# Kernel tuning notes

Hardware: AMD Instinct MI355X
Metric: run time of the kernel (lower is better)

Reference implementation:

```python
import jax, jax.numpy as jnp
import numpy as np

N_NODES = 100000
N_EDGES = 640000
IN_CH, HID_CH, OUT_CH = 256, 128, 64


def setup_inputs() -> dict:
    key = jax.random.key(0)
    ks = jax.random.split(key, 6)
    x = jax.random.normal(ks[0], (N_NODES, IN_CH), dtype=jnp.float32)
    edge_index = jax.random.randint(ks[1], (2, N_EDGES), 0, N_NODES, dtype=jnp.int32)
    # Glorot-style init for GCNConv weights
    W1 = jax.random.normal(ks[2], (IN_CH, HID_CH), dtype=jnp.float32) * (1.0 / np.sqrt(IN_CH))
    W_mu = jax.random.normal(ks[3], (HID_CH, OUT_CH), dtype=jnp.float32) * (1.0 / np.sqrt(HID_CH))
    W_logvar = jax.random.normal(ks[4], (HID_CH, OUT_CH), dtype=jnp.float32) * (1.0 / np.sqrt(HID_CH))
    return {
        "x": x,
        "edge_index": edge_index,
        "W1": W1,
        "b1": jnp.zeros((HID_CH,), jnp.float32),
        "W_mu": W_mu,
        "b_mu": jnp.zeros((OUT_CH,), jnp.float32),
        "W_logvar": W_logvar,
        "b_logvar": jnp.zeros((OUT_CH,), jnp.float32),
    }


def reference(x, edge_index, W1, b1, W_mu, b_mu, W_logvar, b_logvar):
    N = x.shape[0]
    # PyG GCNConv default: add self-loops, symmetric normalization D^-1/2 A_hat D^-1/2
    loops = jnp.arange(N, dtype=edge_index.dtype)
    src = jnp.concatenate([edge_index[0], loops])  # [E+N]
    dst = jnp.concatenate([edge_index[1], loops])  # [E+N]
    deg = jax.ops.segment_sum(jnp.ones_like(src, dtype=x.dtype), dst, num_segments=N)
    dinv = jax.lax.rsqrt(deg)  # deg >= 1 due to self-loops
    norm = dinv[src] * dinv[dst]  # [E+N]

    def gcn_conv(h, W, b):
        h = h @ W                                   # [N, d_out]
        msg = h[src] * norm[:, None]                # gather + scale  [E+N, d_out]
        out = jax.ops.segment_sum(msg, dst, num_segments=N)  # scatter-add
        return out + b

    h = jax.nn.relu(gcn_conv(x, W1, b1))
    mu = gcn_conv(h, W_mu, b_mu)
    logvar = gcn_conv(h, W_logvar, b_logvar)
    return (mu, logvar)
```

## Files before the change

### kernel.cpp

```cpp
#include <hip/hip_runtime.h>
#include <hip/hip_bf16.h>

#define N_NODES 100000
#define E_EDGES 640000

typedef __attribute__((ext_vector_type(8))) short short8;
typedef __attribute__((ext_vector_type(4))) float float4v;

__device__ __forceinline__ float bf2f(unsigned int u16) {
    union { unsigned int i; float f; } c; c.i = u16 << 16; return c.f;
}
__device__ __forceinline__ unsigned short f2bf(float f) {
    union { float f; unsigned int i; } c; c.f = f;
    unsigned int x = c.i;
    unsigned int r = (x + 0x7fffu + ((x >> 16) & 1u)) >> 16;
    return (unsigned short)r;
}

#define ASYNC16(g, l)                                                          \
    __builtin_amdgcn_global_load_lds(                                          \
        (const __attribute__((address_space(1))) void*)(g),                    \
        (__attribute__((address_space(3))) void*)(l), 16, 0, 0)

#define WS_HIST    0
#define WS_CURSOR  524288
#define WS_OFFS    1048576
#define WS_DINV    1572864
#define WS_BSUMS   2097152
#define WS_EIDX    2621440
#define WS_WP1     7864320
#define WS_WP2     7929856
#define WS_H0      7962624
#define WS_H       33562624

__global__ __launch_bounds__(256) void k_hist(const int* __restrict__ dst, int* __restrict__ hist) {
    int e = blockIdx.x * 256 + threadIdx.x;
    if (e < E_EDGES) atomicAdd(&hist[dst[e]], 1);
}

__global__ __launch_bounds__(256) void k_scan1(const int* __restrict__ hist,
                                               int* __restrict__ offs,
                                               int* __restrict__ bsums,
                                               float* __restrict__ dinv) {
    __shared__ int sd[256];
    int t = threadIdx.x;
    int base = blockIdx.x * 1024 + t * 4;
    int v[4];
#pragma unroll
    for (int j = 0; j < 4; ++j) v[j] = (base + j < N_NODES) ? hist[base + j] : 0;
#pragma unroll
    for (int j = 0; j < 4; ++j)
        if (base + j < N_NODES) dinv[base + j] = rsqrtf((float)(v[j] + 1));
    int s = v[0] + v[1] + v[2] + v[3];
    sd[t] = s;
    __syncthreads();
    for (int d = 1; d < 256; d <<= 1) {
        int x = (t >= d) ? sd[t - d] : 0;
        __syncthreads();
        sd[t] += x;
        __syncthreads();
    }
    int excl = sd[t] - s;
    if (t == 255) bsums[blockIdx.x] = sd[255];
    int run = excl;
#pragma unroll
    for (int j = 0; j < 4; ++j) {
        if (base + j < N_NODES) offs[base + j] = run;
        run += v[j];
    }
}

__global__ __launch_bounds__(128) void k_scan2(int* __restrict__ bsums, int nb) {
    __shared__ int sd[128];
    int t = threadIdx.x;
    int v = (t < nb) ? bsums[t] : 0;
    sd[t] = v;
    __syncthreads();
    for (int d = 1; d < 128; d <<= 1) {
        int x = (t >= d) ? sd[t - d] : 0;
        __syncthreads();
        sd[t] += x;
        __syncthreads();
    }
    if (t < nb) bsums[t] = sd[t] - v;
}

__global__ __launch_bounds__(256) void k_scan3(int* __restrict__ offs, const int* __restrict__ bsums) {
    int i = blockIdx.x * 256 + threadIdx.x;
    if (i < N_NODES) offs[i] += bsums[i >> 10];
}

__global__ __launch_bounds__(256) void k_fill(const int* __restrict__ src, const int* __restrict__ dst,
                                              const int* __restrict__ offs, int* __restrict__ cursor,
                                              const float* __restrict__ dinv,
                                              int2* __restrict__ eidx) {
    int e = blockIdx.x * 256 + threadIdx.x;
    if (e < E_EDGES) {
        int s = src[e], d = dst[e];
        int p = offs[d] + atomicAdd(&cursor[d], 1);
        int2 v;
        v.x = s;
        v.y = __float_as_int(dinv[s] * dinv[d]);
        eidx[p] = v;
    }
}

__global__ __launch_bounds__(256) void k_pack(const float* __restrict__ W1,
                                              const float* __restrict__ Wmu,
                                              const float* __restrict__ Wlv,
                                              unsigned short* __restrict__ Wp1,
                                              unsigned short* __restrict__ Wp2) {
    int i = blockIdx.x * 256 + threadIdx.x;
    if (i < 256 * 128) {
        int k = i >> 7, n = i & 127;
        Wp1[n * 256 + k] = f2bf(W1[i]);
    }
    if (i < 128 * 128) {
        int k = i >> 7, n = i & 127;
        float w = (n < 64) ? Wmu[k * 64 + n] : Wlv[k * 64 + (n - 64)];
        Wp2[n * 128 + k] = f2bf(w);
    }
}

__global__ __launch_bounds__(256) void k_mgemm1(const float* __restrict__ A,
                                                const unsigned short* __restrict__ Bpack,
                                                unsigned short* __restrict__ out) {
    __shared__ float As[128 * 32];
    __shared__ unsigned short Bs[128 * 40];
    int tid = threadIdx.x;
    int row0 = blockIdx.x * 128;
    int wave = tid >> 6, lane = tid & 63;
    int c = lane & 15, q = lane >> 4;
    int wrow = (wave >> 1) * 64, wcol = (wave & 1) * 64;

    float4v acc[4][4];
#pragma unroll
    for (int i = 0; i < 4; ++i)
#pragma unroll
        for (int j = 0; j < 4; ++j) acc[i][j] = (float4v){0.f, 0.f, 0.f, 0.f};

    int srow = tid >> 1;
    int shalf = (tid & 1) * 16;

    for (int k0 = 0; k0 < 256; k0 += 32) {
        const unsigned short* bsrc = Bpack + (size_t)srow * 256 + k0 + shalf;
        short8 b0 = *(const short8*)(bsrc);
        short8 b1 = *(const short8*)(bsrc + 8);
#pragma unroll
        for (int t = 0; t < 4; ++t) {
            int S = (t * 4 + wave) * 64 + lane;
            int row = S >> 3, j = S & 7;
            int kq = j ^ (row & 7);
            const float* g = A + (size_t)(row0 + row) * 256 + k0 + kq * 4;
            float* ldst = As + (t * 4 + wave) * 256;
            if (row0 + row < N_NODES) ASYNC16(g, ldst);
        }
        *(short8*)(&Bs[srow * 40 + shalf])     = b0;
        *(short8*)(&Bs[srow * 40 + shalf + 8]) = b1;
        __syncthreads();

        short8 af[4], bfr[4];
#pragma unroll
        for (int mt = 0; mt < 4; ++mt) {
            int r = wrow + mt * 16 + c;
            int j0 = (q * 2) ^ (r & 7);
            float4v fa = *(const float4v*)(&As[r * 32 + j0 * 4]);
            float4v fb = *(const float4v*)(&As[r * 32 + (j0 ^ 1) * 4]);
            short8 s;
#pragma unroll
            for (int jj = 0; jj < 4; ++jj) s[jj]     = (short)f2bf(fa[jj]);
#pragma unroll
            for (int jj = 0; jj < 4; ++jj) s[4 + jj] = (short)f2bf(fb[jj]);
            af[mt] = s;
        }
#pragma unroll
        for (int nt = 0; nt < 4; ++nt)
            bfr[nt] = *(const short8*)(&Bs[(wcol + nt * 16 + c) * 40 + q * 8]);
#pragma unroll
        for (int mt = 0; mt < 4; ++mt)
#pragma unroll
            for (int nt = 0; nt < 4; ++nt)
                acc[mt][nt] = __builtin_amdgcn_mfma_f32_16x16x32_bf16(af[mt], bfr[nt], acc[mt][nt], 0, 0, 0);
        __syncthreads();
    }

#pragma unroll
    for (int mt = 0; mt < 4; ++mt) {
#pragma unroll
        for (int i = 0; i < 4; ++i) {
            int row = row0 + wrow + mt * 16 + q * 4 + i;
            if (row >= N_NODES) continue;
#pragma unroll
            for (int nt = 0; nt < 4; ++nt) {
                int cc = wcol + nt * 16 + c;
                out[(size_t)row * 128 + cc] = f2bf(acc[mt][nt][i]);
            }
        }
    }
}

__global__ __launch_bounds__(256) void k_mgemm2(const unsigned short* __restrict__ A,
                                                const unsigned short* __restrict__ Bpack,
                                                const float* __restrict__ bias0,
                                                const float* __restrict__ bias1,
                                                float* __restrict__ out) {
    constexpr int LDT = 40;
    __shared__ unsigned short As[128 * LDT];
    __shared__ unsigned short Bs[128 * LDT];
    int tid = threadIdx.x;
    int row0 = blockIdx.x * 128;
    int wave = tid >> 6, lane = tid & 63;
    int c = lane & 15, q = lane >> 4;
    int wrow = (wave >> 1) * 64, wcol = (wave & 1) * 64;

    float4v acc[4][4];
#pragma unroll
    for (int i = 0; i < 4; ++i)
#pragma unroll
        for (int j = 0; j < 4; ++j) acc[i][j] = (float4v){0.f, 0.f, 0.f, 0.f};

    int srow = tid >> 1, shalf = (tid & 1) * 16;
    const short8 zed = {0, 0, 0, 0, 0, 0, 0, 0};

    for (int k0 = 0; k0 < 128; k0 += 32) {
        const unsigned short* bsrc = Bpack + (size_t)srow * 128 + k0 + shalf;
        short8 b0 = *(const short8*)(bsrc);
        short8 b1 = *(const short8*)(bsrc + 8);
        int grow = row0 + srow;
        short8 a0 = zed, a1 = zed;
        if (grow < N_NODES) {
            const unsigned short* asrc = A + (size_t)grow * 128 + k0 + shalf;
            a0 = *(const short8*)(asrc);
            a1 = *(const short8*)(asrc + 8);
        }
        *(short8*)(&Bs[srow * LDT + shalf])     = b0;
        *(short8*)(&Bs[srow * LDT + shalf + 8]) = b1;
        *(short8*)(&As[srow * LDT + shalf])     = a0;
        *(short8*)(&As[srow * LDT + shalf + 8]) = a1;
        __syncthreads();

        short8 af[4], bfr[4];
#pragma unroll
        for (int mt = 0; mt < 4; ++mt)
            af[mt] = *(const short8*)(&As[(wrow + mt * 16 + c) * LDT + q * 8]);
#pragma unroll
        for (int nt = 0; nt < 4; ++nt)
            bfr[nt] = *(const short8*)(&Bs[(wcol + nt * 16 + c) * LDT + q * 8]);
#pragma unroll
        for (int mt = 0; mt < 4; ++mt)
#pragma unroll
            for (int nt = 0; nt < 4; ++nt)
                acc[mt][nt] = __builtin_amdgcn_mfma_f32_16x16x32_bf16(af[mt], bfr[nt], acc[mt][nt], 0, 0, 0);
        __syncthreads();
    }

#pragma unroll
    for (int mt = 0; mt < 4; ++mt) {
#pragma unroll
        for (int i = 0; i < 4; ++i) {
            int row = row0 + wrow + mt * 16 + q * 4 + i;
            if (row >= N_NODES) continue;
#pragma unroll
            for (int nt = 0; nt < 4; ++nt) {
                int cc = wcol + nt * 16 + c;
                float v = acc[mt][nt][i];
                if (cc < 64) out[(size_t)row * 64 + cc] = v + bias0[cc];
                else out[(size_t)N_NODES * 64 + (size_t)row * 64 + (cc - 64)] = v + bias1[cc - 64];
            }
        }
    }
}

template <int BIAS_RELU>
__global__ __launch_bounds__(256) void k_agg(const unsigned int* __restrict__ in,
                                             unsigned int* __restrict__ out,
                                             const float* __restrict__ dinv,
                                             const int2* __restrict__ eidx,
                                             const int* __restrict__ offs,
                                             const int* __restrict__ cnt,
                                             const float* __restrict__ bias) {
    int wid = (blockIdx.x * 256 + threadIdx.x) >> 6;
    if (wid >= N_NODES) return;
    int l = threadIdx.x & 63;
    float di = dinv[wid];
    unsigned int u = in[(size_t)wid * 64 + l];
    float sc = di * di;
    float ax = sc * bf2f(u & 0xffffu);
    float ay = sc * bf2f(u >> 16);
    if (BIAS_RELU) { ax += bias[2 * l]; ay += bias[2 * l + 1]; }
    int start = offs[wid];
    int n = cnt[wid];

    for (int base = 0; base < n; base += 64) {
        int m = min(n - base, 64);
        int sreg = 0; float wreg = 0.f;
        if (l < m) {
            int2 ev = eidx[start + base + l];
            sreg = ev.x;
            wreg = __int_as_float(ev.y);
        }
        int e = 0;
        for (; e + 4 <= m; e += 4) {
            int s0 = __shfl(sreg, e),     s1 = __shfl(sreg, e + 1);
            int s2 = __shfl(sreg, e + 2), s3 = __shfl(sreg, e + 3);
            float w0 = __shfl(wreg, e),     w1 = __shfl(wreg, e + 1);
            float w2 = __shfl(wreg, e + 2), w3 = __shfl(wreg, e + 3);
            unsigned int u0 = in[(size_t)s0 * 64 + l];
            unsigned int u1 = in[(size_t)s1 * 64 + l];
            unsigned int u2 = in[(size_t)s2 * 64 + l];
            unsigned int u3 = in[(size_t)s3 * 64 + l];
            ax += w0 * bf2f(u0 & 0xffffu); ay += w0 * bf2f(u0 >> 16);
            ax += w1 * bf2f(u1 & 0xffffu); ay += w1 * bf2f(u1 >> 16);
            ax += w2 * bf2f(u2 & 0xffffu); ay += w2 * bf2f(u2 >> 16);
            ax += w3 * bf2f(u3 & 0xffffu); ay += w3 * bf2f(u3 >> 16);
        }
        for (; e < m; ++e) {
            int s0 = __shfl(sreg, e);
            float w0 = __shfl(wreg, e);
            unsigned int u0 = in[(size_t)s0 * 64 + l];
            ax += w0 * bf2f(u0 & 0xffffu); ay += w0 * bf2f(u0 >> 16);
        }
    }
    if (BIAS_RELU) { ax = fmaxf(ax, 0.f); ay = fmaxf(ay, 0.f); }
    out[(size_t)wid * 64 + l] = (unsigned int)f2bf(ax) | ((unsigned int)f2bf(ay) << 16);
}

extern "C" void kernel_launch(void* const* d_in, const int* in_sizes, int n_in,
                              void* d_out, int out_size, void* d_ws, size_t ws_size,
                              hipStream_t stream) {
    const float* x    = (const float*)d_in[0];
    const int*   ei   = (const int*)d_in[1];
    const float* W1   = (const float*)d_in[2];
    const float* b1   = (const float*)d_in[3];
    const float* Wmu  = (const float*)d_in[4];
    const float* bmu  = (const float*)d_in[5];
    const float* Wlv  = (const float*)d_in[6];
    const float* blv  = (const float*)d_in[7];
    float* outp = (float*)d_out;

    const int* src = ei;
    const int* dst = ei + E_EDGES;

    char* ws = (char*)d_ws;
    int*            hist   = (int*)(ws + WS_HIST);
    int*            cursor = (int*)(ws + WS_CURSOR);
    int*            offs   = (int*)(ws + WS_OFFS);
    float*          dinv   = (float*)(ws + WS_DINV);
    int*            bsums  = (int*)(ws + WS_BSUMS);
    int2*           eidx   = (int2*)(ws + WS_EIDX);
    unsigned short* Wp1    = (unsigned short*)(ws + WS_WP1);
    unsigned short* Wp2    = (unsigned short*)(ws + WS_WP2);
    unsigned short* h0     = (unsigned short*)(ws + WS_H0);
    unsigned short* h      = (unsigned short*)(ws + WS_H);

    const int NB_N = (N_NODES + 255) / 256;
    const int NB_E = (E_EDGES + 255) / 256;
    const int NB_S = (N_NODES + 1023) / 1024;
    const int NB_G = (N_NODES + 127) / 128;

    hipMemsetAsync(ws + WS_HIST, 0, 1048576, stream);
    k_hist<<<NB_E, 256, 0, stream>>>(dst, hist);
    k_scan1<<<NB_S, 256, 0, stream>>>(hist, offs, bsums, dinv);
    k_scan2<<<1, 128, 0, stream>>>(bsums, NB_S);
    k_scan3<<<NB_N, 256, 0, stream>>>(offs, bsums);
    k_fill<<<NB_E, 256, 0, stream>>>(src, dst, offs, cursor, dinv, eidx);
    k_pack<<<128, 256, 0, stream>>>(W1, Wmu, Wlv, Wp1, Wp2);

    k_mgemm1<<<NB_G, 256, 0, stream>>>(x, Wp1, h0);
    k_agg<1><<<(N_NODES * 64 + 255) / 256, 256, 0, stream>>>(
        (const unsigned int*)h0, (unsigned int*)h, dinv, eidx, offs, hist, b1);

    k_agg<0><<<(N_NODES * 64 + 255) / 256, 256, 0, stream>>>(
        (const unsigned int*)h, (unsigned int*)h0, dinv, eidx, offs, hist, nullptr);
    k_mgemm2<<<NB_G, 256, 0, stream>>>(h0, Wp2, bmu, blv, outp);
}
```

Measured before the change: 361.6 us.

## Drop LDS staging in GEMMs and fold scan fixup into consumers

Both MFMA GEMM kernels no longer stage A and B tiles in shared memory. Each wave now loads its own 32 rows of A and the full B fragments straight from global memory into registers, which removes the block barriers and LDS traffic. The small B matrix is read by every wave and is expected to stay in cache. The separate scan-fixup kernel is removed, and the block-sum offset is added where offsets are read in fill and aggregation, saving one launch and one pass over the offsets array. The cost is more global/L2 load traffic for B and for the non-coalesced A row reads.

```diff
diff --git a/kernel.cpp b/kernel.cpp
--- a/kernel.cpp
+++ b/kernel.cpp
@@ -16,11 +16,6 @@
     unsigned int r = (x + 0x7fffu + ((x >> 16) & 1u)) >> 16;
     return (unsigned short)r;
 }
-
-#define ASYNC16(g, l)                                                          \
-    __builtin_amdgcn_global_load_lds(                                          \
-        (const __attribute__((address_space(1))) void*)(g),                    \
-        (__attribute__((address_space(3))) void*)(l), 16, 0, 0)
 
 #define WS_HIST    0
 #define WS_CURSOR  524288
@@ -85,19 +80,15 @@
     if (t < nb) bsums[t] = sd[t] - v;
 }
 
-__global__ __launch_bounds__(256) void k_scan3(int* __restrict__ offs, const int* __restrict__ bsums) {
-    int i = blockIdx.x * 256 + threadIdx.x;
-    if (i < N_NODES) offs[i] += bsums[i >> 10];
-}
-
 __global__ __launch_bounds__(256) void k_fill(const int* __restrict__ src, const int* __restrict__ dst,
-                                              const int* __restrict__ offs, int* __restrict__ cursor,
+                                              const int* __restrict__ offs, const int* __restrict__ bsums,
+                                              int* __restrict__ cursor,
                                               const float* __restrict__ dinv,
                                               int2* __restrict__ eidx) {
     int e = blockIdx.x * 256 + threadIdx.x;
     if (e < E_EDGES) {
         int s = src[e], d = dst[e];
-        int p = offs[d] + atomicAdd(&cursor[d], 1);
+        int p = offs[d] + bsums[d >> 10] + atomicAdd(&cursor[d], 1);
         int2 v;
         v.x = s;
         v.y = __float_as_int(dinv[s] * dinv[d]);
@@ -125,76 +116,59 @@
 __global__ __launch_bounds__(256) void k_mgemm1(const float* __restrict__ A,
                                                 const unsigned short* __restrict__ Bpack,
                                                 unsigned short* __restrict__ out) {
-    __shared__ float As[128 * 32];
-    __shared__ unsigned short Bs[128 * 40];
     int tid = threadIdx.x;
-    int row0 = blockIdx.x * 128;
     int wave = tid >> 6, lane = tid & 63;
     int c = lane & 15, q = lane >> 4;
-    int wrow = (wave >> 1) * 64, wcol = (wave & 1) * 64;
-
-    float4v acc[4][4];
-#pragma unroll
-    for (int i = 0; i < 4; ++i)
-#pragma unroll
-        for (int j = 0; j < 4; ++j) acc[i][j] = (float4v){0.f, 0.f, 0.f, 0.f};
-
-    int srow = tid >> 1;
-    int shalf = (tid & 1) * 16;
-
+    int row0 = blockIdx.x * 128 + wave * 32;
+
+    float4v acc[2][8];
+#pragma unroll
+    for (int i = 0; i < 2; ++i)
+#pragma unroll
+        for (int j = 0; j < 8; ++j) acc[i][j] = (float4v){0.f, 0.f, 0.f, 0.f};
+
+    const float* a0 = A + (size_t)(row0 + c) * 256;
+    const float* a1 = A + (size_t)(row0 + 16 + c) * 256;
+    bool v0 = (row0 + c) < N_NODES;
+    bool v1 = (row0 + 16 + c) < N_NODES;
+    const float4v z4 = {0.f, 0.f, 0.f, 0.f};
+
+#pragma unroll 2
     for (int k0 = 0; k0 < 256; k0 += 32) {
-        const unsigned short* bsrc = Bpack + (size_t)srow * 256 + k0 + shalf;
-        short8 b0 = *(const short8*)(bsrc);
-        short8 b1 = *(const short8*)(bsrc + 8);
-#pragma unroll
-        for (int t = 0; t < 4; ++t) {
-            int S = (t * 4 + wave) * 64 + lane;
-            int row = S >> 3, j = S & 7;
-            int kq = j ^ (row & 7);
-            const float* g = A + (size_t)(row0 + row) * 256 + k0 + kq * 4;
-            float* ldst = As + (t * 4 + wave) * 256;
-            if (row0 + row < N_NODES) ASYNC16(g, ldst);
-        }
-        *(short8*)(&Bs[srow * 40 + shalf])     = b0;
-        *(short8*)(&Bs[srow * 40 + shalf + 8]) = b1;
-        __syncthreads();
-
-        short8 af[4], bfr[4];
-#pragma unroll
-        for (int mt = 0; mt < 4; ++mt) {
-            int r = wrow + mt * 16 + c;
-            int j0 = (q * 2) ^ (r & 7);
-            float4v fa = *(const float4v*)(&As[r * 32 + j0 * 4]);
-            float4v fb = *(const float4v*)(&As[r * 32 + (j0 ^ 1) * 4]);
-            short8 s;
-#pragma unroll
-            for (int jj = 0; jj < 4; ++jj) s[jj]     = (short)f2bf(fa[jj]);
-#pragma unroll
-            for (int jj = 0; jj < 4; ++jj) s[4 + jj] = (short)f2bf(fb[jj]);
-            af[mt] = s;
-        }
-#pragma unroll
-        for (int nt = 0; nt < 4; ++nt)
-            bfr[nt] = *(const short8*)(&Bs[(wcol + nt * 16 + c) * 40 + q * 8]);
-#pragma unroll
-        for (int mt = 0; mt < 4; ++mt)
-#pragma unroll
-            for (int nt = 0; nt < 4; ++nt)
-                acc[mt][nt] = __builtin_amdgcn_mfma_f32_16x16x32_bf16(af[mt], bfr[nt], acc[mt][nt], 0, 0, 0);
-        __syncthreads();
-    }
-
-#pragma unroll
-    for (int mt = 0; mt < 4; ++mt) {
+        int ko = k0 + q * 8;
+        float4v fa0 = v0 ? *(const float4v*)(a0 + ko)     : z4;
+        float4v fb0 = v0 ? *(const float4v*)(a0 + ko + 4) : z4;
+        float4v fa1 = v1 ? *(const float4v*)(a1 + ko)     : z4;
+        float4v fb1 = v1 ? *(const float4v*)(a1 + ko + 4) : z4;
+        short8 bfr[8];
+#pragma unroll
+        for (int nt = 0; nt < 8; ++nt)
+            bfr[nt] = *(const short8*)(Bpack + (size_t)(nt * 16 + c) * 256 + ko);
+        short8 af0, af1;
+#pragma unroll
+        for (int j = 0; j < 4; ++j) af0[j]     = (short)f2bf(fa0[j]);
+#pragma unroll
+        for (int j = 0; j < 4; ++j) af0[4 + j] = (short)f2bf(fb0[j]);
+#pragma unroll
+        for (int j = 0; j < 4; ++j) af1[j]     = (short)f2bf(fa1[j]);
+#pragma unroll
+        for (int j = 0; j < 4; ++j) af1[4 + j] = (short)f2bf(fb1[j]);
+#pragma unroll
+        for (int nt = 0; nt < 8; ++nt) {
+            acc[0][nt] = __builtin_amdgcn_mfma_f32_16x16x32_bf16(af0, bfr[nt], acc[0][nt], 0, 0, 0);
+            acc[1][nt] = __builtin_amdgcn_mfma_f32_16x16x32_bf16(af1, bfr[nt], acc[1][nt], 0, 0, 0);
+        }
+    }
+
+#pragma unroll
+    for (int mt = 0; mt < 2; ++mt) {
 #pragma unroll
         for (int i = 0; i < 4; ++i) {
-            int row = row0 + wrow + mt * 16 + q * 4 + i;
+            int row = row0 + mt * 16 + q * 4 + i;
             if (row >= N_NODES) continue;
 #pragma unroll
-            for (int nt = 0; nt < 4; ++nt) {
-                int cc = wcol + nt * 16 + c;
-                out[(size_t)row * 128 + cc] = f2bf(acc[mt][nt][i]);
-            }
+            for (int nt = 0; nt < 8; ++nt)
+                out[(size_t)row * 128 + nt * 16 + c] = f2bf(acc[mt][nt][i]);
         }
     }
 }
@@ -204,65 +178,48 @@
                                                 const float* __restrict__ bias0,
                                                 const float* __restrict__ bias1,
                                                 float* __restrict__ out) {
-    constexpr int LDT = 40;
-    __shared__ unsigned short As[128 * LDT];
-    __shared__ unsigned short Bs[128 * LDT];
     int tid = threadIdx.x;
-    int row0 = blockIdx.x * 128;
     int wave = tid >> 6, lane = tid & 63;
     int c = lane & 15, q = lane >> 4;
-    int wrow = (wave >> 1) * 64, wcol = (wave & 1) * 64;
-
-    float4v acc[4][4];
-#pragma unroll
-    for (int i = 0; i < 4; ++i)
-#pragma unroll
-        for (int j = 0; j < 4; ++j) acc[i][j] = (float4v){0.f, 0.f, 0.f, 0.f};
-
-    int srow = tid >> 1, shalf = (tid & 1) * 16;
-    const short8 zed = {0, 0, 0, 0, 0, 0, 0, 0};
-
+    int row0 = blockIdx.x * 128 + wave * 32;
+
+    float4v acc[2][8];
+#pragma unroll
+    for (int i = 0; i < 2; ++i)
+#pragma unroll
+        for (int j = 0; j < 8; ++j) acc[i][j] = (float4v){0.f, 0.f, 0.f, 0.f};
+
+    const unsigned short* a0 = A + (size_t)(row0 + c) * 128;
+    const unsigned short* a1 = A + (size_t)(row0 + 16 + c) * 128;
+    bool v0 = (row0 + c) < N_NODES;
+    bool v1 = (row0 + 16 + c) < N_NODES;
+    const short8 z8 = {0, 0, 0, 0, 0, 0, 0, 0};
+
+#pragma unroll 2
     for (int k0 = 0; k0 < 128; k0 += 32) {
-        const unsigned short* bsrc = Bpack + (size_t)srow * 128 + k0 + shalf;
-        short8 b0 = *(const short8*)(bsrc);
-        short8 b1 = *(const short8*)(bsrc + 8);
-        int grow = row0 + srow;
-        short8 a0 = zed, a1 = zed;
-        if (grow < N_NODES) {
-            const unsigned short* asrc = A + (size_t)grow * 128 + k0 + shalf;
-            a0 = *(const short8*)(asrc);
-            a1 = *(const short8*)(asrc + 8);
-        }
-        *(short8*)(&Bs[srow * LDT + shalf])     = b0;
-        *(short8*)(&Bs[srow * LDT + shalf + 8]) = b1;
-        *(short8*)(&As[srow * LDT + shalf])     = a0;
-        *(short8*)(&As[srow * LDT + shalf + 8]) = a1;
-        __syncthreads();
-
-        short8 af[4], bfr[4];
-#pragma unroll
-        for (int mt = 0; mt < 4; ++mt)
-            af[mt] = *(const short8*)(&As[(wrow + mt * 16 + c) * LDT + q * 8]);
-#pragma unroll
-        for (int nt = 0; nt < 4; ++nt)
-            bfr[nt] = *(const short8*)(&Bs[(wcol + nt * 16 + c) * LDT + q * 8]);
-#pragma unroll
-        for (int mt = 0; mt < 4; ++mt)
-#pragma unroll
-            for (int nt = 0; nt < 4; ++nt)
-                acc[mt][nt] = __builtin_amdgcn_mfma_f32_16x16x32_bf16(af[mt], bfr[nt], acc[mt][nt], 0, 0, 0);
-        __syncthreads();
-    }
-
-#pragma unroll
-    for (int mt = 0; mt < 4; ++mt) {
+        int ko = k0 + q * 8;
+        short8 af0 = v0 ? *(const short8*)(a0 + ko) : z8;
+        short8 af1 = v1 ? *(const short8*)(a1 + ko) : z8;
+        short8 bfr[8];
+#pragma unroll
+        for (int nt = 0; nt < 8; ++nt)
+            bfr[nt] = *(const short8*)(Bpack + (size_t)(nt * 16 + c) * 128 + ko);
+#pragma unroll
+        for (int nt = 0; nt < 8; ++nt) {
+            acc[0][nt] = __builtin_amdgcn_mfma_f32_16x16x32_bf16(af0, bfr[nt], acc[0][nt], 0, 0, 0);
+            acc[1][nt] = __builtin_amdgcn_mfma_f32_16x16x32_bf16(af1, bfr[nt], acc[1][nt], 0, 0, 0);
+        }
+    }
+
+#pragma unroll
+    for (int mt = 0; mt < 2; ++mt) {
 #pragma unroll
         for (int i = 0; i < 4; ++i) {
-            int row = row0 + wrow + mt * 16 + q * 4 + i;
+            int row = row0 + mt * 16 + q * 4 + i;
             if (row >= N_NODES) continue;
 #pragma unroll
-            for (int nt = 0; nt < 4; ++nt) {
-                int cc = wcol + nt * 16 + c;
+            for (int nt = 0; nt < 8; ++nt) {
+                int cc = nt * 16 + c;
                 float v = acc[mt][nt][i];
                 if (cc < 64) out[(size_t)row * 64 + cc] = v + bias0[cc];
                 else out[(size_t)N_NODES * 64 + (size_t)row * 64 + (cc - 64)] = v + bias1[cc - 64];
@@ -277,6 +234,7 @@
                                              const float* __restrict__ dinv,
                                              const int2* __restrict__ eidx,
                                              const int* __restrict__ offs,
+                                             const int* __restrict__ bsums,
                                              const int* __restrict__ cnt,
                                              const float* __restrict__ bias) {
     int wid = (blockIdx.x * 256 + threadIdx.x) >> 6;
@@ -288,7 +246,7 @@
     float ax = sc * bf2f(u & 0xffffu);
     float ay = sc * bf2f(u >> 16);
     if (BIAS_RELU) { ax += bias[2 * l]; ay += bias[2 * l + 1]; }
-    int start = offs[wid];
+    int start = offs[wid] + bsums[wid >> 10];
     int n = cnt[wid];
 
     for (int base = 0; base < n; base += 64) {
@@ -353,7 +311,6 @@
     unsigned short* h0     = (unsigned short*)(ws + WS_H0);
     unsigned short* h      = (unsigned short*)(ws + WS_H);
 
-    const int NB_N = (N_NODES + 255) / 256;
     const int NB_E = (E_EDGES + 255) / 256;
     const int NB_S = (N_NODES + 1023) / 1024;
     const int NB_G = (N_NODES + 127) / 128;
@@ -362,15 +319,14 @@
     k_hist<<<NB_E, 256, 0, stream>>>(dst, hist);
     k_scan1<<<NB_S, 256, 0, stream>>>(hist, offs, bsums, dinv);
     k_scan2<<<1, 128, 0, stream>>>(bsums, NB_S);
-    k_scan3<<<NB_N, 256, 0, stream>>>(offs, bsums);
-    k_fill<<<NB_E, 256, 0, stream>>>(src, dst, offs, cursor, dinv, eidx);
+    k_fill<<<NB_E, 256, 0, stream>>>(src, dst, offs, bsums, cursor, dinv, eidx);
     k_pack<<<128, 256, 0, stream>>>(W1, Wmu, Wlv, Wp1, Wp2);
 
     k_mgemm1<<<NB_G, 256, 0, stream>>>(x, Wp1, h0);
     k_agg<1><<<(N_NODES * 64 + 255) / 256, 256, 0, stream>>>(
-        (const unsigned int*)h0, (unsigned int*)h, dinv, eidx, offs, hist, b1);
+        (const unsigned int*)h0, (unsigned int*)h, dinv, eidx, offs, bsums, hist, b1);
 
     k_agg<0><<<(N_NODES * 64 + 255) / 256, 256, 0, stream>>>(
-        (const unsigned int*)h, (unsigned int*)h0, dinv, eidx, offs, hist, nullptr);
+        (const unsigned int*)h, (unsigned int*)h0, dinv, eidx, offs, bsums, hist, nullptr);
     k_mgemm2<<<NB_G, 256, 0, stream>>>(h0, Wp2, bmu, blv, outp);
 }
```

New measurement: 378.3 us. 1.05x slower.
